# Optimization experiments

Hardware: AMD Instinct MI355X
Metric: run time of the kernel (lower is better)

## Reference

```python
import jax, jax.numpy as jnp
import numpy as np

B, S, T = 64, 48, 48
E, H = 512, 1024
V_SRC, V_TGT = 32000, 32000
PAD = 0


def setup_inputs() -> dict:
    key = jax.random.key(0)
    ks = jax.random.split(key, 24)
    def g(k, shape, scale=0.05):
        return jax.random.normal(k, shape, dtype=jnp.float32) * scale
    return {
        "src_ids": jax.random.randint(ks[0], (S, B), 0, V_SRC),
        "tgt_ids": jax.random.randint(ks[1], (T, B), 0, V_TGT),
        "src_lengths": S,
        "src_emb": g(ks[2], (V_SRC, E)).at[PAD].set(0.0),
        "tgt_emb": g(ks[3], (V_TGT, E)).at[PAD].set(0.0),
        "cnn_w": g(ks[4], (E, E, 2)),
        "cnn_b": g(ks[5], (E,)),
        "enc_Wih_f": g(ks[6], (4 * H, E)),
        "enc_Whh_f": g(ks[7], (4 * H, H)),
        "enc_bih_f": g(ks[8], (4 * H,)),
        "enc_bhh_f": g(ks[9], (4 * H,)),
        "enc_Wih_b": g(ks[10], (4 * H, E)),
        "enc_Whh_b": g(ks[11], (4 * H, H)),
        "enc_bih_b": g(ks[12], (4 * H,)),
        "enc_bhh_b": g(ks[13], (4 * H,)),
        "dec_Wih": g(ks[14], (4 * H, E + H)),
        "dec_Whh": g(ks[15], (4 * H, H)),
        "dec_bih": g(ks[16], (4 * H,)),
        "dec_bhh": g(ks[17], (4 * H,)),
        "Wh": g(ks[18], (H, 2 * H)),
        "Wc": g(ks[19], (H, 2 * H)),
        "Watt": g(ks[20], (H, 2 * H)),
        "Wcomb": g(ks[21], (H, 3 * H)),
        "Wvocab": g(ks[22], (V_TGT, H)),
    }


def _lstm_cell(x, h, c, Wih, Whh, bih, bhh):
    gates = x @ Wih.T + h @ Whh.T + bih + bhh  # (b, 4h)
    i, f, g, o = jnp.split(gates, 4, axis=-1)
    c_new = jax.nn.sigmoid(f) * c + jax.nn.sigmoid(i) * jnp.tanh(g)
    h_new = jax.nn.sigmoid(o) * jnp.tanh(c_new)
    return h_new, c_new


def _forward(src_ids, tgt_ids,
             src_emb, tgt_emb, cnn_w, cnn_b,
             enc_Wih_f, enc_Whh_f, enc_bih_f, enc_bhh_f,
             enc_Wih_b, enc_Whh_b, enc_bih_b, enc_bhh_b,
             dec_Wih, dec_Whh, dec_bih, dec_bhh,
             Wh, Wc, Watt, Wcomb, Wvocab):
    b = src_ids.shape[1]
    h = Wh.shape[0]
    # ---- encode ----
    X = src_emb[src_ids]                       # (S, b, E)
    Xc = jnp.transpose(X, (1, 2, 0))           # (b, E, S)
    # Conv1d kernel_size=2, padding='same' in torch pads (left=0, right=1)
    Xc = jax.lax.conv_general_dilated(Xc, cnn_w, window_strides=(1,),
                                      padding=[(0, 1)],
                                      dimension_numbers=("NCH", "OIH", "NCH"))
    Xc = Xc + cnn_b[None, :, None]
    X = jnp.transpose(Xc, (2, 0, 1))           # (S, b, E)

    h0 = jnp.zeros((b, h), dtype=X.dtype)
    def fstep(carry, x_t):
        hh, cc = carry
        hh, cc = _lstm_cell(x_t, hh, cc, enc_Wih_f, enc_Whh_f, enc_bih_f, enc_bhh_f)
        return (hh, cc), hh
    def bstep(carry, x_t):
        hh, cc = carry
        hh, cc = _lstm_cell(x_t, hh, cc, enc_Wih_b, enc_Whh_b, enc_bih_b, enc_bhh_b)
        return (hh, cc), hh
    (hf, cf), out_f = jax.lax.scan(fstep, (h0, h0), X)
    (hb, cb), out_b = jax.lax.scan(bstep, (h0, h0), X[::-1])
    out_b = out_b[::-1]
    enc_hiddens = jnp.concatenate([out_f, out_b], axis=-1)   # (S, b, 2h)
    enc_hiddens = jnp.transpose(enc_hiddens, (1, 0, 2))      # (b, S, 2h)
    dec_h = jnp.concatenate([hf, hb], axis=1) @ Wh.T         # (b, h)
    dec_c = jnp.concatenate([cf, cb], axis=1) @ Wc.T         # (b, h)

    # ---- decode ----
    enc_proj = enc_hiddens @ Watt.T            # (b, S, h)
    enc_mask = jnp.zeros((b, enc_hiddens.shape[1]), dtype=bool)  # all full length
    Y = tgt_emb[tgt_ids[:-1]]                  # (T-1, b, E)

    def dstep(carry, Y_t):
        hh, cc, o_prev = carry
        ybar = jnp.concatenate([o_prev, Y_t], axis=1)        # (b, h+E)
        hh, cc = _lstm_cell(ybar, hh, cc, dec_Wih, dec_Whh, dec_bih, dec_bhh)
        e_t = jnp.einsum("bh,bsh->bs", hh, enc_proj)
        e_t = jnp.where(enc_mask, -jnp.inf, e_t)
        alpha = jax.nn.softmax(e_t, axis=-1)
        a_t = jnp.einsum("bs,bsd->bd", alpha, enc_hiddens)   # (b, 2h)
        O_t = jnp.tanh(jnp.concatenate([a_t, hh], axis=1) @ Wcomb.T)  # dropout rate 0
        return (hh, cc, O_t), O_t

    o0 = jnp.zeros((b, h), dtype=X.dtype)
    _, combined = jax.lax.scan(dstep, (dec_h, dec_c, o0), Y)  # (T-1, b, h)

    P = jax.nn.log_softmax(combined @ Wvocab.T, axis=-1)      # (T-1, b, V)
    gold = tgt_ids[1:]                                        # (T-1, b)
    logp = jnp.take_along_axis(P, gold[..., None], axis=-1)[..., 0]
    tmask = (gold != PAD).astype(P.dtype)
    return (logp * tmask).sum(axis=0)                         # (b,)


def reference(src_ids, tgt_ids, src_lengths,
              src_emb, tgt_emb, cnn_w, cnn_b,
              enc_Wih_f, enc_Whh_f, enc_bih_f, enc_bhh_f,
              enc_Wih_b, enc_Whh_b, enc_bih_b, enc_bhh_b,
              dec_Wih, dec_Whh, dec_bih, dec_bhh,
              Wh, Wc, Watt, Wcomb, Wvocab):
    # src_lengths == S for every sentence (packed seq degenerates to full-length LSTM)
    return _forward(src_ids, tgt_ids, src_emb, tgt_emb, cnn_w, cnn_b,
                    enc_Wih_f, enc_Whh_f, enc_bih_f, enc_bhh_f,
                    enc_Wih_b, enc_Whh_b, enc_bih_b, enc_bhh_b,
                    dec_Wih, dec_Whh, dec_bih, dec_bhh,
                    Wh, Wc, Watt, Wcomb, Wvocab)
```

## Files before the change

### kernel.cpp

```cpp
#include <hip/hip_runtime.h>
#include <hip/hip_bf16.h>
#include <math.h>

using f32x4 = __attribute__((ext_vector_type(4))) float;
using s16x8 = __attribute__((ext_vector_type(8))) short;
typedef unsigned short u16;
typedef unsigned int u32;
typedef unsigned long long u64;

#define MFMA16(a,b,c) __builtin_amdgcn_mfma_f32_16x16x32_bf16(a,b,c,0,0,0)
#define SCOPE_A __HIP_MEMORY_SCOPE_AGENT
#define FP 16

__device__ __forceinline__ float bf2f(u16 u){
  union { u32 i; float f; } v; v.i = ((u32)u) << 16; return v.f;
}
__device__ __forceinline__ u16 f2bf(float f){
  union { float f; u32 i; } v; v.f = f;
  u32 x = v.i;
  return (u16)((x + 0x7fffu + ((x >> 16) & 1u)) >> 16);
}
__device__ __forceinline__ float sigm(float x){ return 1.0f/(1.0f + expf(-x)); }

__device__ __forceinline__ s16x8 pack8(const float* p){
  s16x8 r;
  #pragma unroll
  for (int i = 0; i < 8; ++i) r[i] = (short)f2bf(p[i]);
  return r;
}

__device__ __forceinline__ void coh_st32(void* p, u32 v){
  __hip_atomic_store((u32*)p, v, __ATOMIC_RELAXED, SCOPE_A);
}
__device__ __forceinline__ float u2f(u32 u){ union { u32 i; float f; } v; v.i = u; return v.f; }
__device__ __forceinline__ u32 f2u(float f){ union { float f; u32 i; } v; v.f = f; return v.i; }

__device__ __forceinline__ void poll(const int* flags, int n, int gen){
  for (int i = threadIdx.x; i < n; i += 256)
    while (__hip_atomic_load(flags + i*FP, __ATOMIC_RELAXED, SCOPE_A) < gen)
      __builtin_amdgcn_s_sleep(1);
  __syncthreads();
}
__device__ __forceinline__ void setflag(int* flag, int gen){
  __syncthreads();
  if (threadIdx.x == 0)
    __hip_atomic_store(flag, gen, __ATOMIC_RELAXED, SCOPE_A);
}

__device__ __forceinline__ void gemm_k1024(
    const u16* ap, const char* wb0, const char* wb1, int xo, int addb,
    f32x4& a0, f32x4& a1)
{
  #pragma unroll
  for (int c = 0; c < 2; ++c){
    s16x8 st[16];
    #pragma unroll
    for (int q = 0; q < 16; ++q) st[q] = *(const s16x8*)(ap + c*512 + q*32);
    #pragma unroll
    for (int q = 0; q < 16; ++q){
      int cb = (addb + (c*512 + q*32)*2) ^ xo;
      a0 = MFMA16(st[q], *(const s16x8*)(wb0 + cb), a0);
      a1 = MFMA16(st[q], *(const s16x8*)(wb1 + cb), a1);
    }
  }
}

__global__ void k_zero(float* __restrict__ p, long n){
  long i = (long)blockIdx.x*blockDim.x + threadIdx.x;
  long st = (long)gridDim.x*blockDim.x;
  for (; i < n; i += st) p[i] = 0.0f;
}

__global__ void k_cast_bf16(const float* __restrict__ src, u16* __restrict__ dst, long n){
  long i = ((long)blockIdx.x*blockDim.x + threadIdx.x)*4;
  long st = (long)gridDim.x*blockDim.x*4;
  for (; i < n; i += st){
    float4 v = *(const float4*)(src + i);
    *(ushort4*)(dst + i) = make_ushort4(f2bf(v.x), f2bf(v.y), f2bf(v.z), f2bf(v.w));
  }
}

__global__ void k_addv(const float* __restrict__ a, const float* __restrict__ b,
                       float* __restrict__ d, int n){
  int i = blockIdx.x*blockDim.x + threadIdx.x;
  if (i < n) d[i] = a[i] + b[i];
}

__global__ void k_repack_conv(const float* __restrict__ w, u16* __restrict__ dst){
  int i = blockIdx.x*256 + threadIdx.x;
  int o = i >> 9, ii = i & 511;
  dst[(size_t)o*1024 + ii]       = f2bf(w[((size_t)o*512 + ii)*2 + 0]);
  dst[(size_t)o*1024 + 512 + ii] = f2bf(w[((size_t)o*512 + ii)*2 + 1]);
}

__global__ void k_build_wy(const float* __restrict__ dWih, u16* __restrict__ Wy){
  int i = blockIdx.x*256 + threadIdx.x;
  int r = i >> 9, c = i & 511;
  Wy[(size_t)r*512 + c] = f2bf(dWih[(size_t)r*1536 + 1024 + c]);
}

__global__ void k_split_wcomb(const float* __restrict__ Wcomb,
                              u16* __restrict__ Wca, u16* __restrict__ Whp){
  int r = blockIdx.x;
  for (int c = threadIdx.x; c < 2048; c += 256)
    Wca[(size_t)r*2048 + c] = f2bf(Wcomb[(size_t)r*3072 + c]);
  for (int c = threadIdx.x; c < 1024; c += 256)
    Whp[(size_t)r*1024 + c] = f2bf(Wcomb[(size_t)r*3072 + 2048 + c]);
}

__global__ void k_gather_src(const int* __restrict__ ids, const float* __restrict__ emb,
                             u16* __restrict__ Aconv){
  int s = blockIdx.x;
  int b = blockIdx.y;
  int e = threadIdx.x*4;
  float4 v = make_float4(0.f,0.f,0.f,0.f);
  if (s < 48){ int id = ids[s*64 + b]; v = *(const float4*)(emb + (size_t)id*512 + e); }
  ushort4 u = make_ushort4(f2bf(v.x), f2bf(v.y), f2bf(v.z), f2bf(v.w));
  if (s < 48) *(ushort4*)(Aconv + ((size_t)(s*64 + b))*1024 + e) = u;
  if (s >= 1) *(ushort4*)(Aconv + ((size_t)((s-1)*64 + b))*1024 + 512 + e) = u;
}

__global__ void k_gather_y(const int* __restrict__ ids, const float* __restrict__ emb,
                           u16* __restrict__ Y){
  int t = blockIdx.x; int b = blockIdx.y; int e = threadIdx.x*4;
  int id = ids[t*64 + b];
  float4 v = *(const float4*)(emb + (size_t)id*512 + e);
  *(ushort4*)(Y + ((size_t)(t*64 + b))*512 + e) = make_ushort4(f2bf(v.x), f2bf(v.y), f2bf(v.z), f2bf(v.w));
}

template<bool OUT_BF16, bool PACKG>
__global__ __launch_bounds__(256) void k_gemm(
    const u16* __restrict__ A0, long lda0,
    const u16* __restrict__ A1, long lda1, int ksplit,
    const u16* __restrict__ W, int K,
    void* __restrict__ Out, long ldc,
    const float* __restrict__ bias)
{
  __shared__ __align__(16) u16 As[64][72];
  __shared__ __align__(16) u16 Ws[64][72];
  const int t = threadIdx.x;
  const int m0 = blockIdx.x*64, n0 = blockIdx.y*64;
  const int w = t >> 6, l = t & 63, lr = l & 15, lh = l >> 4;
  const int sr = t >> 2, sk = (t & 3) << 4;

  f32x4 acc[4] = {{0,0,0,0},{0,0,0,0},{0,0,0,0},{0,0,0,0}};

  for (int kc = 0; kc < K; kc += 64){
    {
      const u16* wp = W + (size_t)(n0 + sr)*K + kc + sk;
      *(s16x8*)&Ws[sr][sk]     = *(const s16x8*)wp;
      *(s16x8*)&Ws[sr][sk + 8] = *(const s16x8*)(wp + 8);
    }
    {
      const u16* ap = (kc < ksplit)
        ? A0 + (size_t)(m0 + sr)*lda0 + kc
        : A1 + (size_t)(m0 + sr)*lda1 + (kc - ksplit);
      ap += sk;
      *(s16x8*)&As[sr][sk]     = *(const s16x8*)ap;
      *(s16x8*)&As[sr][sk + 8] = *(const s16x8*)(ap + 8);
    }
    __syncthreads();
    #pragma unroll
    for (int kk = 0; kk < 64; kk += 32){
      s16x8 a = *(const s16x8*)&As[w*16 + lr][kk + lh*8];
      #pragma unroll
      for (int ct = 0; ct < 4; ++ct){
        s16x8 bfr = *(const s16x8*)&Ws[ct*16 + lr][kk + lh*8];
        acc[ct] = MFMA16(a, bfr, acc[ct]);
      }
    }
    __syncthreads();
  }
  #pragma unroll
  for (int ct = 0; ct < 4; ++ct){
    #pragma unroll
    for (int rr = 0; rr < 4; ++rr){
      long row = m0 + w*16 + lh*4 + rr;
      long col = n0 + ct*16 + lr;
      float v = acc[ct][rr];
      if (bias) v += bias[col];
      if (PACKG){
        long time = row >> 6, b = row & 63, g = col >> 10, j = col & 1023;
        ((u16*)Out)[((time*1024 + j)*4 + g)*64 + b] = f2bf(v);
      } else {
        long oi = row*ldc + col;
        if (OUT_BF16) ((u16*)Out)[oi] = f2bf(v);
        else          ((float*)Out)[oi] = v;
      }
    }
  }
}

__global__ __launch_bounds__(256) void k_enc_persist(
    const float* __restrict__ WhhF, const float* __restrict__ WhhB,
    const u16* __restrict__ GfP, const u16* __restrict__ GbP,
    u16* __restrict__ hEF, u16* __restrict__ hEB,
    const u16* __restrict__ hzero,
    float* __restrict__ cF, float* __restrict__ cB,
    u16* __restrict__ Aatt, u16* __restrict__ cfbf, u16* __restrict__ cbbf,
    int* Eflags,
    const u16* __restrict__ Ybf, const u16* __restrict__ WyBf,
    const float* __restrict__ bdec, u16* __restrict__ GyP,
    const float* __restrict__ Wv, u16* __restrict__ WvBf)
{
  extern __shared__ char smem[];
  const int t = threadIdx.x, blk = blockIdx.x;
  const int w = t >> 6, l = t & 63, lr = l & 15, lh = l >> 4;

  if (blk >= 128){
    const int hb = blk - 128;
    u16 (*As)[72] = (u16(*)[72])smem;
    u16 (*Ws)[72] = (u16(*)[72])(smem + 64*72*2);
    const int sr = t >> 2, sk = (t & 3) << 4;
    for (int tile = hb; tile < 47*64; tile += 128){
      int m0 = (tile % 47)*64, n0 = (tile / 47)*64;
      f32x4 acc[4] = {{0,0,0,0},{0,0,0,0},{0,0,0,0},{0,0,0,0}};
      for (int kc = 0; kc < 512; kc += 64){
        const u16* wp = WyBf + (size_t)(n0 + sr)*512 + kc + sk;
        *(s16x8*)&Ws[sr][sk]     = *(const s16x8*)wp;
        *(s16x8*)&Ws[sr][sk + 8] = *(const s16x8*)(wp + 8);
        const u16* ap = Ybf + (size_t)(m0 + sr)*512 + kc + sk;
        *(s16x8*)&As[sr][sk]     = *(const s16x8*)ap;
        *(s16x8*)&As[sr][sk + 8] = *(const s16x8*)(ap + 8);
        __syncthreads();
        #pragma unroll
        for (int kk = 0; kk < 64; kk += 32){
          s16x8 a = *(const s16x8*)&As[w*16 + lr][kk + lh*8];
          #pragma unroll
          for (int ct = 0; ct < 4; ++ct){
            s16x8 bfr = *(const s16x8*)&Ws[ct*16 + lr][kk + lh*8];
            acc[ct] = MFMA16(a, bfr, acc[ct]);
          }
        }
        __syncthreads();
      }
      #pragma unroll
      for (int ct = 0; ct < 4; ++ct){
        #pragma unroll
        for (int rr = 0; rr < 4; ++rr){
          long row = m0 + w*16 + lh*4 + rr;
          long col = n0 + ct*16 + lr;
          float v = acc[ct][rr] + bdec[col];
          long time = row >> 6, b = row & 63, g = col >> 10, j = col & 1023;
          GyP[((time*1024 + j)*4 + g)*64 + b] = f2bf(v);
        }
      }
    }
    for (long i = ((long)hb*256 + t)*4; i < (long)32000*1024; i += (long)128*256*4){
      float4 v = *(const float4*)(Wv + i);
      *(ushort4*)(WvBf + i) = make_ushort4(f2bf(v.x), f2bf(v.y), f2bf(v.z), f2bf(v.w));
    }
    return;
  }

  const int dir = blk >> 6;
  const int j0 = (blk & 63) << 4;
  const float* Wsrc = dir ? WhhB : WhhF;
  const u16* GP = dir ? GbP : GfP;
  float* c = dir ? cB : cF;
  u16* cobf = dir ? cbbf : cfbf;
  u16* hE = dir ? hEB : hEF;
  int* myflags = Eflags + dir*64*FP;
  const int myidx = blk & 63;

  for (int q = t; q < 64*128; q += 256){
    int row = q >> 7;
    int ck = (q & 127) << 3;
    int wrow = ((row >> 4)*1024) + j0 + (row & 15);
    s16x8 pk = pack8(Wsrc + (size_t)wrow*1024 + ck);
    *(s16x8*)(smem + row*2048 + ((ck*2) ^ ((row & 7) << 4))) = pk;
  }
  __syncthreads();

  const int lane_m = w*16 + lr;
  const int koff = lh*8;
  const char* wp0 = smem + lr*2048;
  const char* wp1 = smem + (16 + lr)*2048;
  const char* wp2 = smem + (32 + lr)*2048;
  const char* wp3 = smem + (48 + lr)*2048;
  const int xo = (lr & 7) << 4;
  const int j = j0 + lr;

  for (int s = 0; s < 48; ++s){
    const u16* hin = s ? (hE + (size_t)(s - 1)*65536) : hzero;
    u16* hout      = hE + (size_t)s*65536;
    const int time = dir ? 47 - s : s;
    if (s) poll(myflags, 64, s);
    f32x4 a0 = {0,0,0,0}, a1 = {0,0,0,0}, a2 = {0,0,0,0}, a3 = {0,0,0,0};
    const u16* ap = hin + (size_t)lane_m*1024 + koff;
    #pragma unroll
    for (int cc = 0; cc < 2; ++cc){
      s16x8 st[16];
      #pragma unroll
      for (int q = 0; q < 16; ++q) st[q] = *(const s16x8*)(ap + cc*512 + q*32);
      #pragma unroll
      for (int q = 0; q < 16; ++q){
        int cb = ((cc*512 + q*32 + koff)*2) ^ xo;
        a0 = MFMA16(st[q], *(const s16x8*)(wp0 + cb), a0);
        a1 = MFMA16(st[q], *(const s16x8*)(wp1 + cb), a1);
        a2 = MFMA16(st[q], *(const s16x8*)(wp2 + cb), a2);
        a3 = MFMA16(st[q], *(const s16x8*)(wp3 + cb), a3);
      }
    }
    #pragma unroll
    for (int rr = 0; rr < 4; ++rr){
      int b = w*16 + lh*4 + rr;
      const u16* gp = GP + (((size_t)time*1024 + j)*4)*64 + b;
      float gi = a0[rr] + bf2f(gp[0]);
      float gf = a1[rr] + bf2f(gp[64]);
      float gg = a2[rr] + bf2f(gp[128]);
      float go = a3[rr] + bf2f(gp[192]);
      float cn = sigm(gf)*c[b*1024 + j] + sigm(gi)*tanhf(gg);
      float hn = sigm(go)*tanhf(cn);
      c[b*1024 + j] = cn;
      u16 hb = f2bf(hn);
      u32 hi2 = __shfl_down((u32)hb, 1);
      if ((lr & 1) == 0)
        coh_st32((u32*)hout + ((b*1024 + j) >> 1), (u32)hb | (hi2 << 16));
      Aatt[((size_t)b*48 + time)*2048 + dir*1024 + j] = hb;
      if (s == 47) cobf[b*1024 + j] = f2bf(cn);
    }
    setflag(myflags + myidx*FP, s + 1);
  }
}

__global__ __launch_bounds__(256) void k_dec_persist(
    const float* __restrict__ dWih, const float* __restrict__ dWhh,
    const u16* __restrict__ GyP,
    const u16* __restrict__ encP, const u16* __restrict__ encWc,
    const u16* __restrict__ Whp,
    const u16* __restrict__ hbinit, u16* __restrict__ hD,
    float* __restrict__ cdec,
    u16* __restrict__ hp, u16* __restrict__ Cbf,
    const u16* __restrict__ obf_zero,
    int* Gflags, int* G2flags, int* Cflags)
{
  extern __shared__ char smem[];
  const int t = threadIdx.x, blk = blockIdx.x;
  const int w = t >> 6, l = t & 63, lr = l & 15, lh = l >> 4;
  const int lane_m = w*16 + lr;
  const int koff = lh*8;
  const int xo = (lr & 7) << 4;

  if (blk < 128){
    const int j0 = blk << 3;
    for (int q = t; q < 32*256; q += 256){
      int row = q >> 8;
      int ck = (q & 255) << 3;
      int wrow = ((row >> 3)*1024) + j0 + (row & 7);
      const float* src = (ck < 1024) ? dWih + (size_t)wrow*1536 + ck
                                     : dWhh + (size_t)wrow*1024 + (ck - 1024);
      s16x8 pk = pack8(src);
      *(s16x8*)(smem + row*4096 + ((ck*2) ^ ((row & 7) << 4))) = pk;
    }
    char* WhpL = smem + 131072;
    for (int q = t; q < 8*128; q += 256){
      int row = q >> 7, ck = (q & 127) << 3;
      s16x8 v = *(const s16x8*)(Whp + (size_t)(j0 + row)*1024 + ck);
      *(s16x8*)(WhpL + row*2048 + ((ck*2) ^ ((row & 7) << 4))) = v;
    }
    __syncthreads();
    const char* wp0 = smem + lr*4096;
    const char* wp1 = smem + (16 + lr)*4096;
    const char* wph = WhpL + (lr & 7)*2048;
    const int jj = lr & 7, gsel = lr >> 3;
    const int j = j0 + jj;

    s16x8 hreg[32];
    {
      const u16* ap = hbinit + (size_t)lane_m*1024 + koff;
      #pragma unroll
      for (int q = 0; q < 32; ++q) hreg[q] = *(const s16x8*)(ap + q*32);
    }

    for (int tt = 0; tt < 47; ++tt){
      u16* hout = hD + (size_t)tt*65536;
      f32x4 a0 = {0,0,0,0}, a1 = {0,0,0,0};
      #pragma unroll
      for (int q = 0; q < 32; ++q){
        int cb = ((1024 + q*32 + koff)*2) ^ xo;
        a0 = MFMA16(hreg[q], *(const s16x8*)(wp0 + cb), a0);
        a1 = MFMA16(hreg[q], *(const s16x8*)(wp1 + cb), a1);
      }
      if (tt) poll(Cflags, 64, tt);
      const u16* Ao = tt ? (Cbf + (size_t)(tt - 1)*65536) : obf_zero;
      gemm_k1024(Ao + (size_t)lane_m*1024 + koff, wp0, wp1, xo, koff*2, a0, a1);
      #pragma unroll
      for (int rr = 0; rr < 4; ++rr){
        float v0 = a0[rr], v1 = a1[rr];
        float p0 = __shfl_xor(v0, 8, 64);
        float p1 = __shfl_xor(v1, 8, 64);
        if (gsel == 0){
          int b = w*16 + lh*4 + rr;
          const u16* gp = GyP + (((size_t)tt*1024 + j)*4)*64 + b;
          float gi = v0 + bf2f(gp[0]);
          float gf = p0 + bf2f(gp[64]);
          float gg = v1 + bf2f(gp[128]);
          float go = p1 + bf2f(gp[192]);
          float cn = sigm(gf)*cdec[b*1024 + j] + sigm(gi)*tanhf(gg);
          float hn = sigm(go)*tanhf(cn);
          cdec[b*1024 + j] = cn;
          u16 hb = f2bf(hn);
          u32 hi2 = __shfl_down((u32)hb, 1);
          if ((jj & 1) == 0)
            coh_st32((u32*)hout + ((b*1024 + j) >> 1), (u32)hb | (hi2 << 16));
        }
      }
      setflag(Gflags + blk*FP, tt + 1);
      poll(Gflags, 128, tt + 1);
      {
        const u16* ap = hout + (size_t)lane_m*1024 + koff;
        #pragma unroll
        for (int q = 0; q < 32; ++q) hreg[q] = *(const s16x8*)(ap + q*32);
      }
      f32x4 hpacc = {0,0,0,0};
      #pragma unroll
      for (int q = 0; q < 32; ++q){
        int cb = ((q*32 + koff)*2) ^ xo;
        s16x8 bw = {0,0,0,0,0,0,0,0};
        if (lr < 8) bw = *(const s16x8*)(wph + cb);
        hpacc = MFMA16(hreg[q], bw, hpacc);
      }
      if (lr < 8){
        u16* hpout = hp + (size_t)tt*65536;
        #pragma unroll
        for (int rr = 0; rr < 4; ++rr){
          u16 hb = f2bf(hpacc[rr]);
          u32 hi2 = __shfl_down((u32)hb, 1);
          if ((lr & 1) == 0)
            coh_st32((u32*)hpout + (((size_t)(w*16 + lh*4 + rr)*1024 + j0 + lr) >> 1),
                     (u32)hb | (hi2 << 16));
        }
      }
      setflag(G2flags + blk*FP, tt + 1);
    }
  } else {
    const int b = blk - 128;
    u16* encPL = (u16*)smem;
    float* hs  = (float*)(smem + 98304);
    float* es  = (float*)(smem + 102400);
    float* al  = es + 48;
    for (int q = t; q < 48*128; q += 256){
      int row = q >> 7, ck = (q & 127) << 3;
      *(s16x8*)&encPL[row*1024 + ck] =
        *(const s16x8*)(encP + ((size_t)b*48 + row)*1024 + ck);
    }
    __syncthreads();

    for (int tt = 0; tt < 47; ++tt){
      poll(Gflags, 128, tt + 1);
      const u16* hrow = hD + (size_t)tt*65536 + (size_t)b*1024;
      {
        ushort4 v4 = ((const ushort4*)hrow)[t];
        hs[4*t]     = bf2f(v4.x);
        hs[4*t + 1] = bf2f(v4.y);
        hs[4*t + 2] = bf2f(v4.z);
        hs[4*t + 3] = bf2f(v4.w);
      }
      __syncthreads();
      for (int s2 = w; s2 < 48; s2 += 4){
        float p = 0.f;
        #pragma unroll
        for (int i = 0; i < 16; ++i)
          p += hs[l + 64*i]*bf2f(encPL[s2*1024 + l + 64*i]);
        #pragma unroll
        for (int d = 32; d >= 1; d >>= 1) p += __shfl_xor(p, d, 64);
        if (l == 0) es[s2] = p;
      }
      __syncthreads();
      if (w == 0){
        float e = (l < 48) ? es[l] : -INFINITY;
        float m = e;
        #pragma unroll
        for (int d = 32; d >= 1; d >>= 1) m = fmaxf(m, __shfl_xor(m, d, 64));
        float ex = (l < 48) ? expf(e - m) : 0.f;
        float su = ex;
        #pragma unroll
        for (int d = 32; d >= 1; d >>= 1) su += __shfl_xor(su, d, 64);
        if (l < 48) al[l] = ex/su;
      }
      __syncthreads();
      poll(G2flags, 128, tt + 1);
      int c0 = t*4;
      ushort4 h4 = *(const ushort4*)(hp + (size_t)tt*65536 + (size_t)b*1024 + c0);
      float acc0 = 0.f, acc1 = 0.f, acc2 = 0.f, acc3 = 0.f;
      const u16* ew = encWc + (size_t)b*48*1024 + c0;
      #pragma unroll 4
      for (int s2 = 0; s2 < 48; ++s2){
        float wgt = al[s2];
        ushort4 e4 = *(const ushort4*)(ew + (size_t)s2*1024);
        acc0 += wgt*bf2f(e4.x); acc1 += wgt*bf2f(e4.y);
        acc2 += wgt*bf2f(e4.z); acc3 += wgt*bf2f(e4.w);
      }
      float v0 = tanhf(bf2f(h4.x) + acc0), v1 = tanhf(bf2f(h4.y) + acc1);
      float v2 = tanhf(bf2f(h4.z) + acc2), v3 = tanhf(bf2f(h4.w) + acc3);
      size_t oi = (size_t)tt*65536 + (size_t)b*1024 + c0;
      coh_st32((u32*)Cbf + (oi >> 1),     (u32)f2bf(v0) | ((u32)f2bf(v1) << 16));
      coh_st32((u32*)Cbf + (oi >> 1) + 1, (u32)f2bf(v2) | ((u32)f2bf(v3) << 16));
      setflag(Cflags + b*FP, tt + 1);
    }
  }
}

#define VNS 25
__global__ __launch_bounds__(256) void k_vocab_lse(
    const u16* __restrict__ Cbf, const u16* __restrict__ Wv, float2* __restrict__ partials)
{
  __shared__ __align__(16) u16 As[128][72];
  __shared__ __align__(16) u16 Bs[128][72];
  __shared__ float2 mg[128][2];
  int rb = blockIdx.x, sp = blockIdx.y;
  int m0 = rb*128;
  int t = threadIdx.x, w = t >> 6, l = t & 63, lr = l & 15, lh = l >> 4;
  int wr = w >> 1, wc = w & 1;
  int sr = t >> 1, sk = (t & 1) << 5;

  float mrun[4][4], srun[4][4];
  #pragma unroll
  for (int m = 0; m < 4; ++m)
    #pragma unroll
    for (int rr = 0; rr < 4; ++rr){ mrun[m][rr] = -INFINITY; srun[m][rr] = 0.f; }

  for (int nt = 0; nt < 10; ++nt){
    int n0 = sp*1280 + nt*128;
    f32x4 acc[4][4];
    #pragma unroll
    for (int m = 0; m < 4; ++m)
      #pragma unroll
      for (int n = 0; n < 4; ++n) acc[m][n] = (f32x4){0,0,0,0};

    for (int kc = 0; kc < 1024; kc += 64){
      int ar = m0 + sr; if (ar > 3007) ar = 3007;
      const u16* ap = Cbf + (size_t)ar*1024 + kc + sk;
      const u16* wp = Wv + (size_t)(n0 + sr)*1024 + kc + sk;
      #pragma unroll
      for (int q = 0; q < 4; ++q){
        *(s16x8*)&As[sr][sk + q*8] = *(const s16x8*)(ap + q*8);
        *(s16x8*)&Bs[sr][sk + q*8] = *(const s16x8*)(wp + q*8);
      }
      __syncthreads();
      #pragma unroll
      for (int kk = 0; kk < 64; kk += 32){
        s16x8 af[4], bf[4];
        #pragma unroll
        for (int m = 0; m < 4; ++m)
          af[m] = *(const s16x8*)&As[wr*64 + m*16 + lr][kk + lh*8];
        #pragma unroll
        for (int n = 0; n < 4; ++n)
          bf[n] = *(const s16x8*)&Bs[wc*64 + n*16 + lr][kk + lh*8];
        #pragma unroll
        for (int m = 0; m < 4; ++m)
          #pragma unroll
          for (int n = 0; n < 4; ++n)
            acc[m][n] = MFMA16(af[m], bf[n], acc[m][n]);
      }
      __syncthreads();
    }
    #pragma unroll
    for (int m = 0; m < 4; ++m){
      #pragma unroll
      for (int rr = 0; rr < 4; ++rr){
        float tm = fmaxf(fmaxf(acc[m][0][rr], acc[m][1][rr]),
                         fmaxf(acc[m][2][rr], acc[m][3][rr]));
        #pragma unroll
        for (int d = 1; d < 16; d <<= 1) tm = fmaxf(tm, __shfl_xor(tm, d, 64));
        float ts = expf(acc[m][0][rr] - tm) + expf(acc[m][1][rr] - tm)
                 + expf(acc[m][2][rr] - tm) + expf(acc[m][3][rr] - tm);
        #pragma unroll
        for (int d = 1; d < 16; d <<= 1) ts += __shfl_xor(ts, d, 64);
        if (tm > mrun[m][rr]){ srun[m][rr] = srun[m][rr]*expf(mrun[m][rr] - tm) + ts; mrun[m][rr] = tm; }
        else srun[m][rr] += ts*expf(tm - mrun[m][rr]);
      }
    }
  }
  __syncthreads();
  if (lr == 0){
    #pragma unroll
    for (int m = 0; m < 4; ++m)
      #pragma unroll
      for (int rr = 0; rr < 4; ++rr)
        mg[wr*64 + m*16 + lh*4 + rr][wc] = make_float2(mrun[m][rr], srun[m][rr]);
  }
  __syncthreads();
  if (t < 128){
    float2 p0 = mg[t][0], p1 = mg[t][1];
    float m = fmaxf(p0.x, p1.x);
    float s = p0.y*expf(p0.x - m) + p1.y*expf(p1.x - m);
    long row = m0 + t;
    if (row < 3008) partials[row*VNS + sp] = make_float2(m, s);
  }
}

__global__ void k_lse(const float2* __restrict__ partials, float* __restrict__ lse){
  int r = blockIdx.x*256 + threadIdx.x;
  if (r >= 3008) return;
  float m = -INFINITY, s = 0.f;
  for (int i = 0; i < VNS; ++i){
    float2 p = partials[r*VNS + i];
    if (p.x > m){ s = s*expf(m - p.x) + p.y; m = p.x; }
    else s += p.y*expf(p.x - m);
  }
  lse[r] = m + logf(s);
}

__global__ __launch_bounds__(256) void k_gold(const u16* __restrict__ Cbf,
                                              const u16* __restrict__ Wv,
                                              const int* __restrict__ tgt,
                                              float* __restrict__ gold){
  int w = threadIdx.x >> 6, l = threadIdx.x & 63;
  int r = blockIdx.x*4 + w;
  int tt = r >> 6, b = r & 63;
  int gid = tgt[(tt + 1)*64 + b];
  const u16* cp = Cbf + (size_t)r*1024;
  const u16* wp = Wv + (size_t)gid*1024;
  float p = 0.f;
  for (int i = l; i < 1024; i += 64) p += bf2f(cp[i])*bf2f(wp[i]);
  for (int d = 32; d >= 1; d >>= 1) p += __shfl_xor(p, d, 64);
  if (l == 0) gold[r] = p;
}

__global__ void k_final(const float* __restrict__ gold, const float* __restrict__ lse,
                        const int* __restrict__ tgt, float* __restrict__ out){
  int b = threadIdx.x;
  if (b >= 64) return;
  float acc = 0.f;
  for (int t = 0; t < 47; ++t){
    int gid = tgt[(t + 1)*64 + b];
    if (gid != 0) acc += gold[t*64 + b] - lse[t*64 + b];
  }
  out[b] = acc;
}

extern "C" void kernel_launch(void* const* d_in, const int* in_sizes, int n_in,
                              void* d_out, int out_size, void* d_ws, size_t ws_size,
                              hipStream_t stream)
{
  (void)in_sizes; (void)n_in; (void)out_size; (void)ws_size;
  const int*   src_ids = (const int*)d_in[0];
  const int*   tgt_ids = (const int*)d_in[1];
  const float* src_emb = (const float*)d_in[3];
  const float* tgt_emb = (const float*)d_in[4];
  const float* cnn_w   = (const float*)d_in[5];
  const float* cnn_b   = (const float*)d_in[6];
  const float* eWih_f  = (const float*)d_in[7];
  const float* eWhh_f  = (const float*)d_in[8];
  const float* ebih_f  = (const float*)d_in[9];
  const float* ebhh_f  = (const float*)d_in[10];
  const float* eWih_b  = (const float*)d_in[11];
  const float* eWhh_b  = (const float*)d_in[12];
  const float* ebih_b  = (const float*)d_in[13];
  const float* ebhh_b  = (const float*)d_in[14];
  const float* dWih    = (const float*)d_in[15];
  const float* dWhh    = (const float*)d_in[16];
  const float* dbih    = (const float*)d_in[17];
  const float* dbhh    = (const float*)d_in[18];
  const float* Wh      = (const float*)d_in[19];
  const float* Wc      = (const float*)d_in[20];
  const float* Watt    = (const float*)d_in[21];
  const float* Wcomb   = (const float*)d_in[22];
  const float* Wvocab  = (const float*)d_in[23];

  char* ws = (char*)d_ws;
  size_t off = 0;
  auto alloc = [&](size_t bytes)->char*{
    char* p = ws + off;
    off = (off + bytes + 255) & ~(size_t)255;
    return p;
  };

  float* cF     = (float*)alloc((size_t)65536*4);
  float* cB     = (float*)alloc((size_t)65536*4);
  u16* obf_zero = (u16*)alloc((size_t)65536*2);
  int* bar      = (int*)alloc(32768);
  size_t zero_floats = ((size_t)262144*2 + 131072 + 32768)/4;
  int* Eflags  = bar;
  int* Gflags  = bar + 2048;
  int* G2flags = bar + 4096;
  int* Cflags  = bar + 6144;

  u16* Wconv_bf = (u16*)alloc((size_t)512*1024*2);
  u16* Wih_f_bf = (u16*)alloc((size_t)4096*512*2);
  u16* Wih_b_bf = (u16*)alloc((size_t)4096*512*2);
  u16* Wy_bf    = (u16*)alloc((size_t)4096*512*2);
  u16* Wh_bf    = (u16*)alloc((size_t)1024*2048*2);
  u16* Wc_bf    = (u16*)alloc((size_t)1024*2048*2);
  u16* Watt_bf  = (u16*)alloc((size_t)1024*2048*2);
  u16* Wca_bf   = (u16*)alloc((size_t)1024*2048*2);
  u16* Whp_bf   = (u16*)alloc((size_t)1024*1024*2);
  u16* Wv_bf    = (u16*)alloc((size_t)32000*1024*2);
  float* benc_f = (float*)alloc(4096*4);
  float* benc_b = (float*)alloc(4096*4);
  float* bdec   = (float*)alloc(4096*4);

  u16* Aconv    = (u16*)alloc((size_t)3072*1024*2);
  u16* Xc       = (u16*)alloc((size_t)3072*512*2);
  u16* GfP      = (u16*)alloc((size_t)48*1024*256*2);
  u16* GbP      = (u16*)alloc((size_t)48*1024*256*2);
  u16* GyP      = (u16*)alloc((size_t)47*1024*256*2);
  u16* Ybf      = (u16*)alloc((size_t)3008*512*2);
  u16* Aatt     = (u16*)alloc((size_t)3072*2048*2);
  u16* encP     = (u16*)alloc((size_t)3072*1024*2);
  u16* encWc    = (u16*)alloc((size_t)3072*1024*2);
  u16* hEF      = (u16*)alloc((size_t)48*65536*2);
  u16* hEB      = (u16*)alloc((size_t)48*65536*2);
  u16* cfbf     = (u16*)alloc((size_t)65536*2);
  u16* cbbf     = (u16*)alloc((size_t)65536*2);
  u16* hbinit   = (u16*)alloc((size_t)65536*2);
  u16* hD       = (u16*)alloc((size_t)47*65536*2);
  float* cdec   = (float*)alloc((size_t)65536*4);
  u16* hp       = (u16*)alloc((size_t)47*65536*2);
  u16* Cbf      = (u16*)alloc((size_t)3008*1024*2);
  float2* partials=(float2*)alloc((size_t)3008*VNS*8);
  float* lse    = (float*)alloc(3008*4);
  float* gold   = (float*)alloc(3008*4);

  k_zero<<<256, 256, 0, stream>>>(cF, (long)zero_floats);

  auto cgrid = [](long n)->int{ long g = (n/4 + 255)/256; return (int)(g > 1024 ? 1024 : g); };
  k_cast_bf16<<<cgrid(4096*512), 256, 0, stream>>>(eWih_f, Wih_f_bf, (long)4096*512);
  k_cast_bf16<<<cgrid(4096*512), 256, 0, stream>>>(eWih_b, Wih_b_bf, (long)4096*512);
  k_cast_bf16<<<cgrid(1024*2048), 256, 0, stream>>>(Wh, Wh_bf, (long)1024*2048);
  k_cast_bf16<<<cgrid(1024*2048), 256, 0, stream>>>(Wc, Wc_bf, (long)1024*2048);
  k_cast_bf16<<<cgrid(1024*2048), 256, 0, stream>>>(Watt, Watt_bf, (long)1024*2048);

  k_addv<<<16, 256, 0, stream>>>(ebih_f, ebhh_f, benc_f, 4096);
  k_addv<<<16, 256, 0, stream>>>(ebih_b, ebhh_b, benc_b, 4096);
  k_addv<<<16, 256, 0, stream>>>(dbih, dbhh, bdec, 4096);

  k_repack_conv<<<1024, 256, 0, stream>>>(cnn_w, Wconv_bf);
  k_build_wy<<<8192, 256, 0, stream>>>(dWih, Wy_bf);
  k_split_wcomb<<<1024, 256, 0, stream>>>(Wcomb, Wca_bf, Whp_bf);

  k_gather_src<<<dim3(49, 64), 128, 0, stream>>>(src_ids, src_emb, Aconv);
  k_gather_y<<<dim3(47, 64), 128, 0, stream>>>(tgt_ids, tgt_emb, Ybf);

  k_gemm<true, false><<<dim3(48, 8), 256, 0, stream>>>(
      Aconv, 1024, Aconv, 1024, 1024, Wconv_bf, 1024, Xc, 512, cnn_b);
  k_gemm<true, true><<<dim3(48, 64), 256, 0, stream>>>(
      Xc, 512, Xc, 512, 512, Wih_f_bf, 512, GfP, 0, benc_f);
  k_gemm<true, true><<<dim3(48, 64), 256, 0, stream>>>(
      Xc, 512, Xc, 512, 512, Wih_b_bf, 512, GbP, 0, benc_b);

  k_enc_persist<<<256, 256, 131072, stream>>>(
      eWhh_f, eWhh_b, GfP, GbP, hEF, hEB, obf_zero, cF, cB,
      Aatt, cfbf, cbbf, Eflags,
      Ybf, Wy_bf, bdec, GyP, Wvocab, Wv_bf);

  k_gemm<true, false><<<dim3(1, 16), 256, 0, stream>>>(
      hEF + (size_t)47*65536, 1024, hEB + (size_t)47*65536, 1024, 1024,
      Wh_bf, 2048, hbinit, 1024, nullptr);
  k_gemm<false, false><<<dim3(1, 16), 256, 0, stream>>>(
      cfbf, 1024, cbbf, 1024, 1024, Wc_bf, 2048, cdec, 1024, nullptr);
  k_gemm<true, false><<<dim3(48, 16), 256, 0, stream>>>(
      Aatt, 2048, Aatt, 2048, 2048, Watt_bf, 2048, encP, 1024, nullptr);
  k_gemm<true, false><<<dim3(48, 16), 256, 0, stream>>>(
      Aatt, 2048, Aatt, 2048, 2048, Wca_bf, 2048, encWc, 1024, nullptr);

  k_dec_persist<<<192, 256, 147456, stream>>>(
      dWih, dWhh, GyP, encP, encWc, Whp_bf, hbinit, hD, cdec,
      hp, Cbf, obf_zero, Gflags, G2flags, Cflags);

  k_vocab_lse<<<dim3(24, VNS), 256, 0, stream>>>(Cbf, Wv_bf, partials);
  k_lse<<<12, 256, 0, stream>>>(partials, lse);
  k_gold<<<752, 256, 0, stream>>>(Cbf, Wv_bf, tgt_ids, gold);
  k_final<<<1, 64, 0, stream>>>(gold, lse, tgt_ids, (float*)d_out);
}
```

Baseline: 2.413 ms.

## Move attention context reduction into gate blocks and repack encWc per j-block

The attention-weighted context sum and tanh combine move from the 64 per-batch attention blocks into the 128 gate blocks. Attention blocks now only publish softmax weights (alphaR) and an Aflags flag. Each gate block reads the alphas into LDS and reduces over its own 8 columns of encWc, which the GEMM now writes in a j-block-major packed layout. This removes the hp global round trip and the G2 barrier, and spreads the context work over more blocks. In exchange it adds extra LDS, per-step alpha loads and a 128-block Cflags poll.

Result: slower. 2.553 ms (+5.8%).

```diff
diff --git a/kernel.cpp b/kernel.cpp
--- a/kernel.cpp
+++ b/kernel.cpp
@@ -128,7 +128,7 @@
   *(ushort4*)(Y + ((size_t)(t*64 + b))*512 + e) = make_ushort4(f2bf(v.x), f2bf(v.y), f2bf(v.z), f2bf(v.w));
 }
 
-template<bool OUT_BF16, bool PACKG>
+template<bool OUT_BF16, bool PACKG, bool PACKE>
 __global__ __launch_bounds__(256) void k_gemm(
     const u16* __restrict__ A0, long lda0,
     const u16* __restrict__ A1, long lda1, int ksplit,
@@ -182,6 +182,10 @@
       if (PACKG){
         long time = row >> 6, b = row & 63, g = col >> 10, j = col & 1023;
         ((u16*)Out)[((time*1024 + j)*4 + g)*64 + b] = f2bf(v);
+      } else if (PACKE){
+        long b = row/48, s = row - b*48;
+        long jblk = col >> 3, jj = col & 7;
+        ((u16*)Out)[(((jblk*48 + s)*64 + b) << 3) + jj] = f2bf(v);
       } else {
         long oi = row*ldc + col;
         if (OUT_BF16) ((u16*)Out)[oi] = f2bf(v);
@@ -327,13 +331,13 @@
 __global__ __launch_bounds__(256) void k_dec_persist(
     const float* __restrict__ dWih, const float* __restrict__ dWhh,
     const u16* __restrict__ GyP,
-    const u16* __restrict__ encP, const u16* __restrict__ encWc,
+    const u16* __restrict__ encP, const u16* __restrict__ encWcP,
     const u16* __restrict__ Whp,
     const u16* __restrict__ hbinit, u16* __restrict__ hD,
     float* __restrict__ cdec,
-    u16* __restrict__ hp, u16* __restrict__ Cbf,
+    float* __restrict__ alphaR, u16* __restrict__ Cbf,
     const u16* __restrict__ obf_zero,
-    int* Gflags, int* G2flags, int* Cflags)
+    int* Gflags, int* Aflags, int* Cflags)
 {
   extern __shared__ char smem[];
   const int t = threadIdx.x, blk = blockIdx.x;
@@ -354,6 +358,8 @@
       *(s16x8*)(smem + row*4096 + ((ck*2) ^ ((row & 7) << 4))) = pk;
     }
     char* WhpL = smem + 131072;
+    float* alphaL = (float*)(smem + 147456);
+    float* hpL    = (float*)(smem + 159744);
     for (int q = t; q < 8*128; q += 256){
       int row = q >> 7, ck = (q & 127) << 3;
       s16x8 v = *(const s16x8*)(Whp + (size_t)(j0 + row)*1024 + ck);
@@ -365,6 +371,7 @@
     const char* wph = WhpL + (lr & 7)*2048;
     const int jj = lr & 7, gsel = lr >> 3;
     const int j = j0 + jj;
+    const int pvb = t & 63, pvj = (t >> 6)*2;
 
     s16x8 hreg[32];
     {
@@ -382,7 +389,7 @@
         a0 = MFMA16(hreg[q], *(const s16x8*)(wp0 + cb), a0);
         a1 = MFMA16(hreg[q], *(const s16x8*)(wp1 + cb), a1);
       }
-      if (tt) poll(Cflags, 64, tt);
+      if (tt) poll(Cflags, 128, tt);
       const u16* Ao = tt ? (Cbf + (size_t)(tt - 1)*65536) : obf_zero;
       gemm_k1024(Ao + (size_t)lane_m*1024 + koff, wp0, wp1, xo, koff*2, a0, a1);
       #pragma unroll
@@ -422,24 +429,37 @@
         hpacc = MFMA16(hreg[q], bw, hpacc);
       }
       if (lr < 8){
-        u16* hpout = hp + (size_t)tt*65536;
-        #pragma unroll
-        for (int rr = 0; rr < 4; ++rr){
-          u16 hb = f2bf(hpacc[rr]);
-          u32 hi2 = __shfl_down((u32)hb, 1);
-          if ((lr & 1) == 0)
-            coh_st32((u32*)hpout + (((size_t)(w*16 + lh*4 + rr)*1024 + j0 + lr) >> 1),
-                     (u32)hb | (hi2 << 16));
+        #pragma unroll
+        for (int rr = 0; rr < 4; ++rr)
+          hpL[(w*16 + lh*4 + rr)*8 + lr] = hpacc[rr];
+      }
+      poll(Aflags, 64, tt + 1);
+      #pragma unroll
+      for (int i = 0; i < 12; ++i)
+        alphaL[t + i*256] = alphaR[(size_t)tt*3072 + t + i*256];
+      __syncthreads();
+      {
+        float ac0 = 0.f, ac1 = 0.f;
+        const u16* ep = encWcP + (size_t)blk*24576 + pvb*8 + pvj;
+        #pragma unroll 4
+        for (int s2 = 0; s2 < 48; ++s2){
+          float wgt = alphaL[pvb*48 + s2];
+          u32 pv2 = *(const u32*)(ep + (size_t)s2*512);
+          ac0 += wgt*bf2f((u16)(pv2 & 0xffff));
+          ac1 += wgt*bf2f((u16)(pv2 >> 16));
         }
-      }
-      setflag(G2flags + blk*FP, tt + 1);
+        float v0 = tanhf(hpL[pvb*8 + pvj]     + ac0);
+        float v1 = tanhf(hpL[pvb*8 + pvj + 1] + ac1);
+        size_t oi = (size_t)tt*65536 + (size_t)pvb*1024 + j0 + pvj;
+        coh_st32((u32*)Cbf + (oi >> 1), (u32)f2bf(v0) | ((u32)f2bf(v1) << 16));
+      }
+      setflag(Cflags + blk*FP, tt + 1);
     }
   } else {
     const int b = blk - 128;
     u16* encPL = (u16*)smem;
     float* hs  = (float*)(smem + 98304);
     float* es  = (float*)(smem + 102400);
-    float* al  = es + 48;
     for (int q = t; q < 48*128; q += 256){
       int row = q >> 7, ck = (q & 127) << 3;
       *(s16x8*)&encPL[row*1024 + ck] =
@@ -477,27 +497,10 @@
         float su = ex;
         #pragma unroll
         for (int d = 32; d >= 1; d >>= 1) su += __shfl_xor(su, d, 64);
-        if (l < 48) al[l] = ex/su;
-      }
-      __syncthreads();
-      poll(G2flags, 128, tt + 1);
-      int c0 = t*4;
-      ushort4 h4 = *(const ushort4*)(hp + (size_t)tt*65536 + (size_t)b*1024 + c0);
-      float acc0 = 0.f, acc1 = 0.f, acc2 = 0.f, acc3 = 0.f;
-      const u16* ew = encWc + (size_t)b*48*1024 + c0;
-      #pragma unroll 4
-      for (int s2 = 0; s2 < 48; ++s2){
-        float wgt = al[s2];
-        ushort4 e4 = *(const ushort4*)(ew + (size_t)s2*1024);
-        acc0 += wgt*bf2f(e4.x); acc1 += wgt*bf2f(e4.y);
-        acc2 += wgt*bf2f(e4.z); acc3 += wgt*bf2f(e4.w);
-      }
-      float v0 = tanhf(bf2f(h4.x) + acc0), v1 = tanhf(bf2f(h4.y) + acc1);
-      float v2 = tanhf(bf2f(h4.z) + acc2), v3 = tanhf(bf2f(h4.w) + acc3);
-      size_t oi = (size_t)tt*65536 + (size_t)b*1024 + c0;
-      coh_st32((u32*)Cbf + (oi >> 1),     (u32)f2bf(v0) | ((u32)f2bf(v1) << 16));
-      coh_st32((u32*)Cbf + (oi >> 1) + 1, (u32)f2bf(v2) | ((u32)f2bf(v3) << 16));
-      setflag(Cflags + b*FP, tt + 1);
+        if (l < 48)
+          coh_st32(&alphaR[(size_t)tt*3072 + b*48 + l], f2u(ex/su));
+      }
+      setflag(Aflags + b*FP, tt + 1);
     }
   }
 }
@@ -675,8 +678,8 @@
   size_t zero_floats = ((size_t)262144*2 + 131072 + 32768)/4;
   int* Eflags  = bar;
   int* Gflags  = bar + 2048;
-  int* G2flags = bar + 4096;
-  int* Cflags  = bar + 6144;
+  int* Aflags  = bar + 4096;
+  int* Cflags  = bar + 5120;
 
   u16* Wconv_bf = (u16*)alloc((size_t)512*1024*2);
   u16* Wih_f_bf = (u16*)alloc((size_t)4096*512*2);
@@ -700,7 +703,7 @@
   u16* Ybf      = (u16*)alloc((size_t)3008*512*2);
   u16* Aatt     = (u16*)alloc((size_t)3072*2048*2);
   u16* encP     = (u16*)alloc((size_t)3072*1024*2);
-  u16* encWc    = (u16*)alloc((size_t)3072*1024*2);
+  u16* encWcP   = (u16*)alloc((size_t)3072*1024*2);
   u16* hEF      = (u16*)alloc((size_t)48*65536*2);
   u16* hEB      = (u16*)alloc((size_t)48*65536*2);
   u16* cfbf     = (u16*)alloc((size_t)65536*2);
@@ -708,7 +711,7 @@
   u16* hbinit   = (u16*)alloc((size_t)65536*2);
   u16* hD       = (u16*)alloc((size_t)47*65536*2);
   float* cdec   = (float*)alloc((size_t)65536*4);
-  u16* hp       = (u16*)alloc((size_t)47*65536*2);
+  float* alphaR = (float*)alloc((size_t)47*3072*4);
   u16* Cbf      = (u16*)alloc((size_t)3008*1024*2);
   float2* partials=(float2*)alloc((size_t)3008*VNS*8);
   float* lse    = (float*)alloc(3008*4);
@@ -734,11 +737,11 @@
   k_gather_src<<<dim3(49, 64), 128, 0, stream>>>(src_ids, src_emb, Aconv);
   k_gather_y<<<dim3(47, 64), 128, 0, stream>>>(tgt_ids, tgt_emb, Ybf);
 
-  k_gemm<true, false><<<dim3(48, 8), 256, 0, stream>>>(
+  k_gemm<true, false, false><<<dim3(48, 8), 256, 0, stream>>>(
       Aconv, 1024, Aconv, 1024, 1024, Wconv_bf, 1024, Xc, 512, cnn_b);
-  k_gemm<true, true><<<dim3(48, 64), 256, 0, stream>>>(
+  k_gemm<true, true, false><<<dim3(48, 64), 256, 0, stream>>>(
       Xc, 512, Xc, 512, 512, Wih_f_bf, 512, GfP, 0, benc_f);
-  k_gemm<true, true><<<dim3(48, 64), 256, 0, stream>>>(
+  k_gemm<true, true, false><<<dim3(48, 64), 256, 0, stream>>>(
       Xc, 512, Xc, 512, 512, Wih_b_bf, 512, GbP, 0, benc_b);
 
   k_enc_persist<<<256, 256, 131072, stream>>>(
@@ -746,19 +749,19 @@
       Aatt, cfbf, cbbf, Eflags,
       Ybf, Wy_bf, bdec, GyP, Wvocab, Wv_bf);
 
-  k_gemm<true, false><<<dim3(1, 16), 256, 0, stream>>>(
+  k_gemm<true, false, false><<<dim3(1, 16), 256, 0, stream>>>(
       hEF + (size_t)47*65536, 1024, hEB + (size_t)47*65536, 1024, 1024,
       Wh_bf, 2048, hbinit, 1024, nullptr);
-  k_gemm<false, false><<<dim3(1, 16), 256, 0, stream>>>(
+  k_gemm<false, false, false><<<dim3(1, 16), 256, 0, stream>>>(
       cfbf, 1024, cbbf, 1024, 1024, Wc_bf, 2048, cdec, 1024, nullptr);
-  k_gemm<true, false><<<dim3(48, 16), 256, 0, stream>>>(
+  k_gemm<true, false, false><<<dim3(48, 16), 256, 0, stream>>>(
       Aatt, 2048, Aatt, 2048, 2048, Watt_bf, 2048, encP, 1024, nullptr);
-  k_gemm<true, false><<<dim3(48, 16), 256, 0, stream>>>(
-      Aatt, 2048, Aatt, 2048, 2048, Wca_bf, 2048, encWc, 1024, nullptr);
-
-  k_dec_persist<<<192, 256, 147456, stream>>>(
-      dWih, dWhh, GyP, encP, encWc, Whp_bf, hbinit, hD, cdec,
-      hp, Cbf, obf_zero, Gflags, G2flags, Cflags);
+  k_gemm<true, false, true><<<dim3(48, 16), 256, 0, stream>>>(
+      Aatt, 2048, Aatt, 2048, 2048, Wca_bf, 2048, encWcP, 1024, nullptr);
+
+  k_dec_persist<<<192, 256, 161792, stream>>>(
+      dWih, dWhh, GyP, encP, encWcP, Whp_bf, hbinit, hD, cdec,
+      alphaR, Cbf, obf_zero, Gflags, Aflags, Cflags);
 
   k_vocab_lse<<<dim3(24, VNS), 256, 0, stream>>>(Cbf, Wv_bf, partials);
   k_lse<<<12, 256, 0, stream>>>(partials, lse);
```

## Overlap vocab log-sum-exp tiles with decoder recurrence via extra persistent blocks

Applied to the files above, without the earlier changes.

Adds 64 extra blocks to the persistent decoder kernel. Each one polls the per-batch context flags and computes vocab GEMM plus partial log-sum-exp tiles as soon as the rows they need are produced. The remaining tiles run in a smaller follow-up vocab kernel. This hides vocab projection work behind the sequential decoder loop, which otherwise leaves many CUs idle. The cost is that the extra blocks compete with the recurrent blocks for CUs and bandwidth. It also relies on all 256 blocks being co-resident, or the spin-polling could deadlock.

Measured after the change: 3.144 ms. 30.3% more time.

```diff
diff --git a/kernel.cpp b/kernel.cpp
--- a/kernel.cpp
+++ b/kernel.cpp
@@ -11,6 +11,7 @@
 #define MFMA16(a,b,c) __builtin_amdgcn_mfma_f32_16x16x32_bf16(a,b,c,0,0,0)
 #define SCOPE_A __HIP_MEMORY_SCOPE_AGENT
 #define FP 16
+#define VNS 25
 
 __device__ __forceinline__ float bf2f(u16 u){
   union { u32 i; float f; } v; v.i = ((u32)u) << 16; return v.f;
@@ -63,6 +64,94 @@
       a1 = MFMA16(st[q], *(const s16x8*)(wb1 + cb), a1);
     }
   }
+}
+
+__device__ __forceinline__ void vocab_tile(
+    const u16* __restrict__ Cbf, const u16* __restrict__ Wv,
+    float2* __restrict__ partials,
+    u16 (*As)[72], u16 (*Bs)[72], float2 (*mg)[2],
+    int rb, int sp)
+{
+  const int t = threadIdx.x, w = t >> 6, l = t & 63, lr = l & 15, lh = l >> 4;
+  const int wr = w >> 1, wc = w & 1;
+  const int sr = t >> 1, sk = (t & 1) << 5;
+  const int m0 = rb*128;
+
+  float mrun[4][4], srun[4][4];
+  #pragma unroll
+  for (int m = 0; m < 4; ++m)
+    #pragma unroll
+    for (int rr = 0; rr < 4; ++rr){ mrun[m][rr] = -INFINITY; srun[m][rr] = 0.f; }
+
+  for (int nt = 0; nt < 10; ++nt){
+    int n0 = sp*1280 + nt*128;
+    f32x4 acc[4][4];
+    #pragma unroll
+    for (int m = 0; m < 4; ++m)
+      #pragma unroll
+      for (int n = 0; n < 4; ++n) acc[m][n] = (f32x4){0,0,0,0};
+
+    for (int kc = 0; kc < 1024; kc += 64){
+      int ar = m0 + sr; if (ar > 3007) ar = 3007;
+      const u16* ap = Cbf + (size_t)ar*1024 + kc + sk;
+      const u16* wp = Wv + (size_t)(n0 + sr)*1024 + kc + sk;
+      #pragma unroll
+      for (int q = 0; q < 4; ++q){
+        *(s16x8*)&As[sr][sk + q*8] = *(const s16x8*)(ap + q*8);
+        *(s16x8*)&Bs[sr][sk + q*8] = *(const s16x8*)(wp + q*8);
+      }
+      __syncthreads();
+      #pragma unroll
+      for (int kk = 0; kk < 64; kk += 32){
+        s16x8 af[4], bf[4];
+        #pragma unroll
+        for (int m = 0; m < 4; ++m)
+          af[m] = *(const s16x8*)&As[wr*64 + m*16 + lr][kk + lh*8];
+        #pragma unroll
+        for (int n = 0; n < 4; ++n)
+          bf[n] = *(const s16x8*)&Bs[wc*64 + n*16 + lr][kk + lh*8];
+        #pragma unroll
+        for (int m = 0; m < 4; ++m)
+          #pragma unroll
+          for (int n = 0; n < 4; ++n)
+            acc[m][n] = MFMA16(af[m], bf[n], acc[m][n]);
+      }
+      __syncthreads();
+    }
+    #pragma unroll
+    for (int m = 0; m < 4; ++m){
+      #pragma unroll
+      for (int rr = 0; rr < 4; ++rr){
+        float tm = fmaxf(fmaxf(acc[m][0][rr], acc[m][1][rr]),
+                         fmaxf(acc[m][2][rr], acc[m][3][rr]));
+        #pragma unroll
+        for (int d = 1; d < 16; d <<= 1) tm = fmaxf(tm, __shfl_xor(tm, d, 64));
+        float ts = expf(acc[m][0][rr] - tm) + expf(acc[m][1][rr] - tm)
+                 + expf(acc[m][2][rr] - tm) + expf(acc[m][3][rr] - tm);
+        #pragma unroll
+        for (int d = 1; d < 16; d <<= 1) ts += __shfl_xor(ts, d, 64);
+        if (tm > mrun[m][rr]){ srun[m][rr] = srun[m][rr]*expf(mrun[m][rr] - tm) + ts; mrun[m][rr] = tm; }
+        else srun[m][rr] += ts*expf(tm - mrun[m][rr]);
+      }
+    }
+  }
+  __syncthreads();
+  if (lr == 0){
+    #pragma unroll
+    for (int m = 0; m < 4; ++m)
+      #pragma unroll
+      for (int rr = 0; rr < 4; ++rr)
+        mg[wr*64 + m*16 + lh*4 + rr][wc] = make_float2(mrun[m][rr], srun[m][rr]);
+  }
+  __syncthreads();
+  if (t < 128){
+    float2 p0 = mg[t][0], p1 = mg[t][1];
+    float m = fmaxf(p0.x, p1.x);
+    float s = p0.y*expf(p0.x - m) + p1.y*expf(p1.x - m);
+    long row = m0 + t;
+    if (row < 3008) partials[row*VNS + sp] = make_float2(m, s);
+  }
+  __syncthreads();
 }
 
 __global__ void k_zero(float* __restrict__ p, long n){
@@ -333,7 +422,8 @@
     float* __restrict__ cdec,
     u16* __restrict__ hp, u16* __restrict__ Cbf,
     const u16* __restrict__ obf_zero,
-    int* Gflags, int* G2flags, int* Cflags)
+    int* Gflags, int* G2flags, int* Cflags,
+    const u16* __restrict__ WvBf, float2* __restrict__ partials)
 {
   extern __shared__ char smem[];
   const int t = threadIdx.x, blk = blockIdx.x;
@@ -434,7 +524,7 @@
       }
       setflag(G2flags + blk*FP, tt + 1);
     }
-  } else {
+  } else if (blk < 192){
     const int b = blk - 128;
     u16* encPL = (u16*)smem;
     float* hs  = (float*)(smem + 98304);
@@ -499,96 +589,29 @@
       coh_st32((u32*)Cbf + (oi >> 1) + 1, (u32)f2bf(v2) | ((u32)f2bf(v3) << 16));
       setflag(Cflags + b*FP, tt + 1);
     }
-  }
-}
-
-#define VNS 25
+  } else {
+    const int v = blk - 192;
+    u16 (*As)[72] = (u16(*)[72])smem;
+    u16 (*Bs)[72] = (u16(*)[72])(smem + 128*72*2);
+    float2 (*mg)[2] = (float2(*)[2])(smem + 2*128*72*2);
+    for (int tile = v*5; tile < v*5 + 5; ++tile){
+      int rb = tile/25, sp = tile - rb*25;
+      poll(Cflags, 64, 2*rb + 2);
+      vocab_tile(Cbf, WvBf, partials, As, Bs, mg, rb, sp);
+    }
+  }
+}
+
 __global__ __launch_bounds__(256) void k_vocab_lse(
-    const u16* __restrict__ Cbf, const u16* __restrict__ Wv, float2* __restrict__ partials)
+    const u16* __restrict__ Cbf, const u16* __restrict__ Wv,
+    float2* __restrict__ partials, int tile0)
 {
   __shared__ __align__(16) u16 As[128][72];
   __shared__ __align__(16) u16 Bs[128][72];
   __shared__ float2 mg[128][2];
-  int rb = blockIdx.x, sp = blockIdx.y;
-  int m0 = rb*128;
-  int t = threadIdx.x, w = t >> 6, l = t & 63, lr = l & 15, lh = l >> 4;
-  int wr = w >> 1, wc = w & 1;
-  int sr = t >> 1, sk = (t & 1) << 5;
-
-  float mrun[4][4], srun[4][4];
-  #pragma unroll
-  for (int m = 0; m < 4; ++m)
-    #pragma unroll
-    for (int rr = 0; rr < 4; ++rr){ mrun[m][rr] = -INFINITY; srun[m][rr] = 0.f; }
-
-  for (int nt = 0; nt < 10; ++nt){
-    int n0 = sp*1280 + nt*128;
-    f32x4 acc[4][4];
-    #pragma unroll
-    for (int m = 0; m < 4; ++m)
-      #pragma unroll
-      for (int n = 0; n < 4; ++n) acc[m][n] = (f32x4){0,0,0,0};
-
-    for (int kc = 0; kc < 1024; kc += 64){
-      int ar = m0 + sr; if (ar > 3007) ar = 3007;
-      const u16* ap = Cbf + (size_t)ar*1024 + kc + sk;
-      const u16* wp = Wv + (size_t)(n0 + sr)*1024 + kc + sk;
-      #pragma unroll
-      for (int q = 0; q < 4; ++q){
-        *(s16x8*)&As[sr][sk + q*8] = *(const s16x8*)(ap + q*8);
-        *(s16x8*)&Bs[sr][sk + q*8] = *(const s16x8*)(wp + q*8);
-      }
-      __syncthreads();
-      #pragma unroll
-      for (int kk = 0; kk < 64; kk += 32){
-        s16x8 af[4], bf[4];
-        #pragma unroll
-        for (int m = 0; m < 4; ++m)
-          af[m] = *(const s16x8*)&As[wr*64 + m*16 + lr][kk + lh*8];
-        #pragma unroll
-        for (int n = 0; n < 4; ++n)
-          bf[n] = *(const s16x8*)&Bs[wc*64 + n*16 + lr][kk + lh*8];
-        #pragma unroll
-        for (int m = 0; m < 4; ++m)
-          #pragma unroll
-          for (int n = 0; n < 4; ++n)
-            acc[m][n] = MFMA16(af[m], bf[n], acc[m][n]);
-      }
-      __syncthreads();
-    }
-    #pragma unroll
-    for (int m = 0; m < 4; ++m){
-      #pragma unroll
-      for (int rr = 0; rr < 4; ++rr){
-        float tm = fmaxf(fmaxf(acc[m][0][rr], acc[m][1][rr]),
-                         fmaxf(acc[m][2][rr], acc[m][3][rr]));
-        #pragma unroll
-        for (int d = 1; d < 16; d <<= 1) tm = fmaxf(tm, __shfl_xor(tm, d, 64));
-        float ts = expf(acc[m][0][rr] - tm) + expf(acc[m][1][rr] - tm)
-                 + expf(acc[m][2][rr] - tm) + expf(acc[m][3][rr] - tm);
-        #pragma unroll
-        for (int d = 1; d < 16; d <<= 1) ts += __shfl_xor(ts, d, 64);
-        if (tm > mrun[m][rr]){ srun[m][rr] = srun[m][rr]*expf(mrun[m][rr] - tm) + ts; mrun[m][rr] = tm; }
-        else srun[m][rr] += ts*expf(tm - mrun[m][rr]);
-      }
-    }
-  }
-  __syncthreads();
-  if (lr == 0){
-    #pragma unroll
-    for (int m = 0; m < 4; ++m)
-      #pragma unroll
-      for (int rr = 0; rr < 4; ++rr)
-        mg[wr*64 + m*16 + lh*4 + rr][wc] = make_float2(mrun[m][rr], srun[m][rr]);
-  }
-  __syncthreads();
-  if (t < 128){
-    float2 p0 = mg[t][0], p1 = mg[t][1];
-    float m = fmaxf(p0.x, p1.x);
-    float s = p0.y*expf(p0.x - m) + p1.y*expf(p1.x - m);
-    long row = m0 + t;
-    if (row < 3008) partials[row*VNS + sp] = make_float2(m, s);
-  }
+  int tile = tile0 + blockIdx.x;
+  int rb = tile/25, sp = tile - rb*25;
+  vocab_tile(Cbf, Wv, partials, As, Bs, mg, rb, sp);
 }
 
 __global__ void k_lse(const float2* __restrict__ partials, float* __restrict__ lse){
@@ -756,11 +779,11 @@
   k_gemm<true, false><<<dim3(48, 16), 256, 0, stream>>>(
       Aatt, 2048, Aatt, 2048, 2048, Wca_bf, 2048, encWc, 1024, nullptr);
 
-  k_dec_persist<<<192, 256, 147456, stream>>>(
+  k_dec_persist<<<256, 256, 147456, stream>>>(
       dWih, dWhh, GyP, encP, encWc, Whp_bf, hbinit, hD, cdec,
-      hp, Cbf, obf_zero, Gflags, G2flags, Cflags);
-
-  k_vocab_lse<<<dim3(24, VNS), 256, 0, stream>>>(Cbf, Wv_bf, partials);
+      hp, Cbf, obf_zero, Gflags, G2flags, Cflags, Wv_bf, partials);
+
+  k_vocab_lse<<<280, 256, 0, stream>>>(Cbf, Wv_bf, partials, 320);
   k_lse<<<12, 256, 0, stream>>>(partials, lse);
   k_gold<<<752, 256, 0, stream>>>(Cbf, Wv_bf, tgt_ids, gold);
   k_final<<<1, 64, 0, stream>>>(gold, lse, tgt_ids, (float*)d_out);
```
